# Kernel optimization log

Hardware: AMD Instinct MI355X
Metric: run time of the kernel (lower is better)

The kernel has to match this reference:

```python
import jax, jax.numpy as jnp
import numpy as np

B, L, H, S, EXP = 8, 2048, 256, 64, 2
E = H * EXP

def setup_inputs() -> dict:
    key = jax.random.key(0)
    ks = jax.random.split(key, 12)
    u = jax.random.normal(ks[0], (B, L, H), dtype=jnp.float32)
    W_in = jax.random.normal(ks[1], (H, 2 * E), dtype=jnp.float32) * 0.02
    b_in = jax.random.normal(ks[2], (2 * E,), dtype=jnp.float32) * 0.02
    conv_w = jax.random.normal(ks[3], (E, 3), dtype=jnp.float32) * 0.3  # depthwise k=3
    conv_b = jax.random.normal(ks[4], (E,), dtype=jnp.float32) * 0.02
    W_x = jax.random.normal(ks[5], (E, 3 * S), dtype=jnp.float32) * 0.02
    b_x = jax.random.normal(ks[6], (3 * S,), dtype=jnp.float32) * 0.02
    A_log = jax.random.normal(ks[7], (S,), dtype=jnp.float32) * 0.1
    Dp = jnp.ones((E,), dtype=jnp.float32)
    W_out = jax.random.normal(ks[8], (E, H), dtype=jnp.float32) * 0.02
    b_out = jax.random.normal(ks[9], (H,), dtype=jnp.float32) * 0.02
    ln_g = jnp.ones((E,), dtype=jnp.float32)
    ln_b = jnp.zeros((E,), dtype=jnp.float32)
    return {"u": u, "W_in": W_in, "b_in": b_in, "conv_w": conv_w, "conv_b": conv_b,
            "W_x": W_x, "b_x": b_x, "A_log": A_log, "Dp": Dp,
            "W_out": W_out, "b_out": b_out, "ln_g": ln_g, "ln_b": ln_b}

def reference(u, W_in, b_in, conv_w, conv_b, W_x, b_x, A_log, Dp, W_out, b_out, ln_g, ln_b):
    Bb, Ll, Hh = u.shape
    Ss = A_log.shape[0]
    Ee = Dp.shape[0]
    xz = u @ W_in + b_in                      # [B,L,2E]
    x, z = jnp.split(xz, 2, axis=-1)          # [B,L,E] each
    # depthwise conv1d, kernel=3, padding=1 along L
    xp = jnp.pad(x, ((0, 0), (1, 1), (0, 0)))
    x = xp[:, :-2] * conv_w[:, 0] + xp[:, 1:-1] * conv_w[:, 1] + xp[:, 2:] * conv_w[:, 2] + conv_b
    x = jax.nn.silu(x)
    ssm = x @ W_x + b_x                       # [B,L,3S]
    delta, Bm, Cm = jnp.split(ssm, 3, axis=-1)
    delta = jax.nn.softplus(delta)            # [B,L,S]
    A = -jnp.exp(jnp.clip(A_log, -5.0, 5.0))  # [S]
    # torch broadcast quirk: delta[...,None] * A[None,None,:] -> [B,L,S,S], entry = delta[b,l,i]*A[j]
    A_d = jnp.exp(jnp.clip(delta[:, :, :, None] * A[None, None, None, :], -10.0, 0.0))  # [B,L,S,S]
    # bmm(B_discrete, x[:,t,:,None]) == (delta*B) * sum_e x, broadcast over E
    inp_term = (delta * Bm) * x.sum(-1, keepdims=True)  # [B,L,S]

    def step(h, inputs):
        A_t, it_t, C_t, x_t = inputs          # [B,S,S],[B,S],[B,S],[B,E]
        h = jnp.einsum('bij,bje->bie', A_t, h) + it_t[:, :, None]
        h = jnp.clip(h, -100.0, 100.0)
        y = jnp.einsum('bse,bs->be', h, C_t) + Dp * x_t
        return h, y

    h0 = jnp.zeros((Bb, Ss, Ee), dtype=u.dtype)
    xs = (jnp.swapaxes(A_d, 0, 1), jnp.swapaxes(inp_term, 0, 1),
          jnp.swapaxes(Cm, 0, 1), jnp.swapaxes(x, 0, 1))
    _, ys = jax.lax.scan(step, h0, xs)
    outputs = jnp.swapaxes(ys, 0, 1)          # [B,L,E]
    mu = outputs.mean(-1, keepdims=True)
    var = ((outputs - mu) ** 2).mean(-1, keepdims=True)
    y = (outputs - mu) / jnp.sqrt(var + 1e-5) * ln_g + ln_b
    y = y * jax.nn.silu(z)
    return y @ W_out + b_out  # dropout is identity in eval mode
```

## Files before the change

### kernel.cpp

```cpp
#include <hip/hip_runtime.h>
#include <hip/hip_bf16.h>

constexpr int BB = 8;
constexpr int LLEN = 2048;
constexpr int HH = 256;
constexpr int EE = 512;
constexpr int MM = BB * LLEN;

typedef short bf16x8 __attribute__((ext_vector_type(8)));
typedef float f32x4  __attribute__((ext_vector_type(4)));

static __device__ inline unsigned short f2bf(float f) {
    unsigned u = __builtin_bit_cast(unsigned, f);
    unsigned r = (u + 0x7FFFu + ((u >> 16) & 1u)) >> 16;
    return (unsigned short)r;
}
static __device__ inline float bf2f(unsigned short h) {
    return __builtin_bit_cast(float, (unsigned)h << 16);
}

#define GL2LDS(gp, lp) __builtin_amdgcn_global_load_lds( \
    (const __attribute__((address_space(1))) void*)(gp), \
    (__attribute__((address_space(3))) void*)(lp), 16, 0, 0)

__global__ __launch_bounds__(256) void cast_bf16_kernel(
    const float* __restrict__ in, unsigned short* __restrict__ out)
{
    int b = blockIdx.x;
    int cpx = gridDim.x >> 3;
    int lin = (b & 7) * cpx + (b >> 3);
    int i = (lin * 256 + threadIdx.x) * 4;
    float4 v = *reinterpret_cast<const float4*>(in + i);
    ushort4 o = {f2bf(v.x), f2bf(v.y), f2bf(v.z), f2bf(v.w)};
    *reinterpret_cast<ushort4*>(out + i) = o;
}

__global__ __launch_bounds__(256) void transpose_cast_kernel(
    const float* __restrict__ W, unsigned short* __restrict__ Wt, int K, int N)
{
    int i = blockIdx.x * 256 + threadIdx.x;
    if (i < K * N) {
        int n = i / K, k = i - n * K;
        Wt[i] = f2bf(W[(size_t)k * N + n]);
    }
}

__global__ __launch_bounds__(256) void k1_gemm(
    const unsigned short* __restrict__ A, const unsigned short* __restrict__ Bt,
    const float* __restrict__ bias,
    unsigned short* __restrict__ xb, unsigned short* __restrict__ zsb)
{
    __shared__ unsigned short Al[128 * 64];
    __shared__ unsigned short Bl[128 * 64];

    const int tid = threadIdx.x;
    const int lane = tid & 63;
    const int wave = tid >> 6;
    const int wrow = wave >> 1, wcol = wave & 1;
    const int l15 = lane & 15;
    const int lk  = lane >> 4;

    const int cpx = gridDim.x >> 3;
    int lin = blockIdx.x;
    lin = (lin & 7) * cpx + (lin >> 3);
    const int row0 = (lin >> 3) * 128;
    const int col0 = (lin & 7) * 128;
    const bool zside = col0 >= EE;
    unsigned short* Cp = zside ? zsb : xb;
    const int cb = zside ? col0 - EE : col0;

    f32x4 acc[4][4] = {};

    #pragma unroll
    for (int t = 0; t < 4; ++t) {
        const int kt = t * 64;
        #pragma unroll
        for (int i = 0; i < 4; ++i) {
            int sid = i * 256 + tid;
            int r = sid >> 3, sl = sid & 7;
            GL2LDS(A + (size_t)(row0 + r) * 256 + kt + ((sl ^ (r & 7)) << 3),
                   &Al[sid * 8]);
        }
        #pragma unroll
        for (int i = 0; i < 4; ++i) {
            int sid = i * 256 + tid;
            int r = sid >> 3, sl = sid & 7;
            GL2LDS(Bt + (size_t)(col0 + r) * 256 + kt + ((sl ^ (r & 7)) << 3),
                   &Bl[sid * 8]);
        }
        asm volatile("s_waitcnt vmcnt(0)" ::: "memory");
        __builtin_amdgcn_sched_barrier(0);
        __builtin_amdgcn_s_barrier();

        bf16x8 af[4][2], bfr[4][2];
        #pragma unroll
        for (int m = 0; m < 4; ++m) {
            const int r = wrow * 64 + m * 16 + l15;
            #pragma unroll
            for (int kk = 0; kk < 2; ++kk) {
                const int sl = (kk * 4 + lk) ^ (r & 7);
                af[m][kk] = *reinterpret_cast<const bf16x8*>(&Al[r * 64 + sl * 8]);
            }
        }
        #pragma unroll
        for (int n = 0; n < 4; ++n) {
            const int r = wcol * 64 + n * 16 + l15;
            #pragma unroll
            for (int kk = 0; kk < 2; ++kk) {
                const int sl = (kk * 4 + lk) ^ (r & 7);
                bfr[n][kk] = *reinterpret_cast<const bf16x8*>(&Bl[r * 64 + sl * 8]);
            }
        }
        #pragma unroll
        for (int kk = 0; kk < 2; ++kk)
            #pragma unroll
            for (int m = 0; m < 4; ++m)
                #pragma unroll
                for (int n = 0; n < 4; ++n)
                    acc[m][n] = __builtin_amdgcn_mfma_f32_16x16x32_bf16(
                        af[m][kk], bfr[n][kk], acc[m][n], 0, 0, 0);

        __builtin_amdgcn_s_barrier();
    }

    #pragma unroll
    for (int m = 0; m < 4; ++m) {
        #pragma unroll
        for (int n = 0; n < 4; ++n) {
            const int colloc = wcol * 64 + n * 16 + l15;
            const float bv = bias[col0 + colloc];
            #pragma unroll
            for (int i = 0; i < 4; ++i) {
                const int row = row0 + wrow * 64 + m * 16 + lk * 4 + i;
                float v = acc[m][n][i] + bv;
                if (zside) v = v / (1.f + __expf(-v));
                Cp[(size_t)row * EE + cb + colloc] = f2bf(v);
            }
        }
    }
}

__global__ __launch_bounds__(256, 1) void kb_mid_gemm3(
    const unsigned short* __restrict__ xb, const unsigned short* __restrict__ zsb,
    const unsigned short* __restrict__ Bt,
    const float* __restrict__ bias, float* __restrict__ out,
    const float* __restrict__ conv_w, const float* __restrict__ conv_b,
    const float* __restrict__ Dp, const float* __restrict__ ln_g,
    const float* __restrict__ ln_b)
{
    __shared__ unsigned short G[64 * 512];
    __shared__ unsigned short Bl[64 * 512];

    const int tid = threadIdx.x;
    const int lane = tid & 63;
    const int wave = tid >> 6;
    const int l15 = lane & 15;
    const int lk  = lane >> 4;

    const int b = blockIdx.x;
    const int lin = (b & 7) * 32 + (b >> 3);
    const int r0 = lin * 64;

    #pragma unroll
    for (int i = 0; i < 16; ++i) {
        int id = i * 256 + tid;
        int r = id >> 6, s = id & 63;
        GL2LDS(Bt + (size_t)r * 512 + ((s ^ (r & 7)) << 3), &Bl[id * 8]);
    }

    const int e0 = lane * 8;
    float cw0[8], cw1[8], cw2[8], cb8[8], dp8[8], lg8[8], lb8[8];
    #pragma unroll
    for (int j = 0; j < 8; ++j) {
        int e = e0 + j;
        cw0[j] = conv_w[e * 3 + 0];
        cw1[j] = conv_w[e * 3 + 1];
        cw2[j] = conv_w[e * 3 + 2];
        cb8[j] = conv_b[e];
        dp8[j] = Dp[e];
        lg8[j] = ln_g[e];
        lb8[j] = ln_b[e];
    }

    for (int it = 0; it < 16; ++it) {
        const int i = wave * 16 + it;
        const int gr = r0 + i;
        const int l = gr & (LLEN - 1);
        const size_t base = (size_t)gr * EE + e0;

        bf16x8 xc = *reinterpret_cast<const bf16x8*>(xb + base);
        bf16x8 xm = {}, xp = {};
        if (l > 0)        xm = *reinterpret_cast<const bf16x8*>(xb + base - EE);
        if (l < LLEN - 1) xp = *reinterpret_cast<const bf16x8*>(xb + base + EE);
        bf16x8 zv = *reinterpret_cast<const bf16x8*>(zsb + base);

        float o[8];
        float s1 = 0.f, s2 = 0.f;
        #pragma unroll
        for (int j = 0; j < 8; ++j) {
            float v = cb8[j]
                    + bf2f((unsigned short)xm[j]) * cw0[j]
                    + bf2f((unsigned short)xc[j]) * cw1[j]
                    + bf2f((unsigned short)xp[j]) * cw2[j];
            float sx = v / (1.f + __expf(-v));
            float oe = dp8[j] * sx;
            o[j] = oe;
            s1 += oe;
            s2 += oe * oe;
        }
        #pragma unroll
        for (int off = 1; off < 64; off <<= 1) {
            s1 += __shfl_xor(s1, off);
            s2 += __shfl_xor(s2, off);
        }
        const float mu  = s1 * (1.f / EE);
        const float var = s2 * (1.f / EE) - mu * mu;
        const float inv = rsqrtf(var + 1e-5f);

        bf16x8 gv;
        #pragma unroll
        for (int j = 0; j < 8; ++j) {
            float gy = ((o[j] - mu) * inv * lg8[j] + lb8[j]) * bf2f((unsigned short)zv[j]);
            gv[j] = (short)f2bf(gy);
        }
        *reinterpret_cast<bf16x8*>(&G[i * 512 + ((lane ^ (i & 7)) << 3)]) = gv;
    }
    __syncthreads();

    const int wrow = wave >> 1, wcol = wave & 1;
    for (int c = 0; c < 4; ++c) {
        f32x4 acc[2][2] = {};
        #pragma unroll
        for (int ks = 0; ks < 16; ++ks) {
            bf16x8 af[2], bfr[2];
            #pragma unroll
            for (int m = 0; m < 2; ++m) {
                const int ra = wrow * 32 + m * 16 + l15;
                const int ph = (ks * 4 + lk) ^ (ra & 7);
                af[m] = *reinterpret_cast<const bf16x8*>(&G[ra * 512 + ph * 8]);
            }
            #pragma unroll
            for (int n = 0; n < 2; ++n) {
                const int rb = wcol * 32 + n * 16 + l15;
                const int ph = (ks * 4 + lk) ^ (rb & 7);
                bfr[n] = *reinterpret_cast<const bf16x8*>(&Bl[rb * 512 + ph * 8]);
            }
            #pragma unroll
            for (int m = 0; m < 2; ++m)
                #pragma unroll
                for (int n = 0; n < 2; ++n)
                    acc[m][n] = __builtin_amdgcn_mfma_f32_16x16x32_bf16(
                        af[m], bfr[n], acc[m][n], 0, 0, 0);
        }
        #pragma unroll
        for (int m = 0; m < 2; ++m) {
            #pragma unroll
            for (int n = 0; n < 2; ++n) {
                int col = c * 64 + wcol * 32 + n * 16 + l15;
                float bv = bias[col];
                #pragma unroll
                for (int i = 0; i < 4; ++i) {
                    int row = r0 + wrow * 32 + m * 16 + lk * 4 + i;
                    out[(size_t)row * HH + col] = acc[m][n][i] + bv;
                }
            }
        }
        if (c < 3) {
            __syncthreads();
            #pragma unroll
            for (int i = 0; i < 16; ++i) {
                int id = i * 256 + tid;
                int r = id >> 6, s = id & 63;
                GL2LDS(Bt + (size_t)((c + 1) * 64 + r) * 512 + ((s ^ (r & 7)) << 3),
                       &Bl[id * 8]);
            }
            __syncthreads();
        }
    }
}

extern "C" void kernel_launch(void* const* d_in, const int* in_sizes, int n_in,
                              void* d_out, int out_size, void* d_ws, size_t ws_size,
                              hipStream_t stream)
{
    const float* u      = (const float*)d_in[0];
    const float* W_in   = (const float*)d_in[1];
    const float* b_in   = (const float*)d_in[2];
    const float* conv_w = (const float*)d_in[3];
    const float* conv_b = (const float*)d_in[4];
    const float* Dp     = (const float*)d_in[8];
    const float* W_out  = (const float*)d_in[9];
    const float* b_out  = (const float*)d_in[10];
    const float* ln_g   = (const float*)d_in[11];
    const float* ln_b   = (const float*)d_in[12];
    float* out = (float*)d_out;

    char* ws = (char*)d_ws;
    unsigned short* ubf   = (unsigned short*)ws; ws += (size_t)MM * HH * 2;
    unsigned short* wtin  = (unsigned short*)ws; ws += (size_t)1024 * HH * 2;
    unsigned short* wtout = (unsigned short*)ws; ws += (size_t)HH * EE * 2;
    unsigned short* xbuf  = (unsigned short*)ws; ws += (size_t)MM * EE * 2;
    unsigned short* zsbuf = (unsigned short*)ws;

    dim3 blk(256);

    transpose_cast_kernel<<<dim3((1024 * HH + 255) / 256), blk, 0, stream>>>(W_in, wtin, HH, 1024);
    transpose_cast_kernel<<<dim3((HH * EE + 255) / 256), blk, 0, stream>>>(W_out, wtout, EE, HH);
    cast_bf16_kernel<<<dim3(MM * HH / 1024), blk, 0, stream>>>(u, ubf);

    k1_gemm<<<dim3(1024), blk, 0, stream>>>(ubf, wtin, b_in, xbuf, zsbuf);

    kb_mid_gemm3<<<dim3(256), blk, 0, stream>>>(
        xbuf, zsbuf, wtout, b_out, out, conv_w, conv_b, Dp, ln_g, ln_b);
}
```

Baseline: 64.97 us.

## Stage GEMM epilogue through LDS and store x/z in column-panel layout

The first GEMM's epilogue now writes its bf16 results into LDS, two 64-row halves at a time, and then emits coalesced 16-byte stores. The global layout of xb and zsb changes from row-major [M,512] to four column panels of [M,128], so each block writes one contiguous panel. The consuming mid kernel is updated to index the panel layout, including the neighbour-row reads for the conv. This replaces scattered 2-byte global stores with wide, coalesced ones, at the cost of extra barriers and an LDS round trip.

```diff
diff --git a/kernel.cpp b/kernel.cpp
--- a/kernel.cpp
+++ b/kernel.cpp
@@ -50,8 +50,9 @@
     const float* __restrict__ bias,
     unsigned short* __restrict__ xb, unsigned short* __restrict__ zsb)
 {
-    __shared__ unsigned short Al[128 * 64];
-    __shared__ unsigned short Bl[128 * 64];
+    __shared__ __align__(16) unsigned short lds[2 * 128 * 64];
+    unsigned short* Al = lds;
+    unsigned short* Bl = lds + 128 * 64;
 
     const int tid = threadIdx.x;
     const int lane = tid & 63;
@@ -66,8 +67,6 @@
     const int row0 = (lin >> 3) * 128;
     const int col0 = (lin & 7) * 128;
     const bool zside = col0 >= EE;
-    unsigned short* Cp = zside ? zsb : xb;
-    const int cb = zside ? col0 - EE : col0;
 
     f32x4 acc[4][4] = {};
 
@@ -123,19 +122,39 @@
         __builtin_amdgcn_s_barrier();
     }
 
+    const int p = (zside ? (col0 - EE) : col0) >> 7;
+    unsigned short* panel = (zside ? zsb : xb) + (size_t)p * ((size_t)MM * 128);
+    unsigned short* Ep = lds;
+
     #pragma unroll
-    for (int m = 0; m < 4; ++m) {
-        #pragma unroll
-        for (int n = 0; n < 4; ++n) {
-            const int colloc = wcol * 64 + n * 16 + l15;
-            const float bv = bias[col0 + colloc];
-            #pragma unroll
-            for (int i = 0; i < 4; ++i) {
-                const int row = row0 + wrow * 64 + m * 16 + lk * 4 + i;
-                float v = acc[m][n][i] + bv;
-                if (zside) v = v / (1.f + __expf(-v));
-                Cp[(size_t)row * EE + cb + colloc] = f2bf(v);
-            }
+    for (int rnd = 0; rnd < 2; ++rnd) {
+        __syncthreads();
+        if (wrow == rnd) {
+            #pragma unroll
+            for (int m = 0; m < 4; ++m) {
+                #pragma unroll
+                for (int n = 0; n < 4; ++n) {
+                    const int colloc = wcol * 64 + n * 16 + l15;
+                    const float bv = bias[col0 + colloc];
+                    #pragma unroll
+                    for (int i = 0; i < 4; ++i) {
+                        const int lrow = m * 16 + lk * 4 + i;
+                        float v = acc[m][n][i] + bv;
+                        if (zside) v = v / (1.f + __expf(-v));
+                        Ep[lrow * 132 + colloc] = f2bf(v);
+                    }
+                }
+            }
+        }
+        __syncthreads();
+        {
+            const int row = tid >> 2, q = tid & 3;
+            const unsigned short* sp = &Ep[row * 132 + q * 32];
+            unsigned short* gp = panel + (size_t)(row0 + rnd * 64 + row) * 128 + q * 32;
+            #pragma unroll
+            for (int j = 0; j < 4; ++j)
+                *reinterpret_cast<bf16x8*>(gp + j * 8) =
+                    *reinterpret_cast<const bf16x8*>(sp + j * 8);
         }
     }
 }
@@ -169,6 +188,8 @@
     }
 
     const int e0 = lane * 8;
+    const size_t pst = (size_t)MM * 128;
+    const size_t poff = (size_t)(lane >> 4) * pst + (e0 & 127);
     float cw0[8], cw1[8], cw2[8], cb8[8], dp8[8], lg8[8], lb8[8];
     #pragma unroll
     for (int j = 0; j < 8; ++j) {
@@ -186,12 +207,12 @@
         const int i = wave * 16 + it;
         const int gr = r0 + i;
         const int l = gr & (LLEN - 1);
-        const size_t base = (size_t)gr * EE + e0;
+        const size_t base = poff + (size_t)gr * 128;
 
         bf16x8 xc = *reinterpret_cast<const bf16x8*>(xb + base);
         bf16x8 xm = {}, xp = {};
-        if (l > 0)        xm = *reinterpret_cast<const bf16x8*>(xb + base - EE);
-        if (l < LLEN - 1) xp = *reinterpret_cast<const bf16x8*>(xb + base + EE);
+        if (l > 0)        xm = *reinterpret_cast<const bf16x8*>(xb + base - 128);
+        if (l < LLEN - 1) xp = *reinterpret_cast<const bf16x8*>(xb + base + 128);
         bf16x8 zv = *reinterpret_cast<const bf16x8*>(zsb + base);
 
         float o[8];
```

After: 76.87 us. 18.3% more time.

## Shrink k1 K-tile and prefetch W_out chunks through registers in output GEMM

Applied to the files above, without the earlier changes.

The first GEMM now steps K in chunks of 32 with unswizzled LDS tiles half the size, using plain __syncthreads instead of the manual barriers. The output GEMM no longer issues direct global-to-LDS loads for W_out. It loads each next chunk into registers while the current chunk's MFMAs run, then writes it into swizzled LDS after a barrier. The goal is to overlap weight fetch with compute and lower LDS use for occupancy. The costs are more registers, more barrier rounds in k1, and possible bank conflicts from the dropped swizzle.

```diff
diff --git a/kernel.cpp b/kernel.cpp
--- a/kernel.cpp
+++ b/kernel.cpp
@@ -50,8 +50,8 @@
     const float* __restrict__ bias,
     unsigned short* __restrict__ xb, unsigned short* __restrict__ zsb)
 {
-    __shared__ unsigned short Al[128 * 64];
-    __shared__ unsigned short Bl[128 * 64];
+    __shared__ unsigned short Al[128 * 32];
+    __shared__ unsigned short Bl[128 * 32];
 
     const int tid = threadIdx.x;
     const int lane = tid & 63;
@@ -72,55 +72,42 @@
     f32x4 acc[4][4] = {};
 
     #pragma unroll
-    for (int t = 0; t < 4; ++t) {
-        const int kt = t * 64;
-        #pragma unroll
-        for (int i = 0; i < 4; ++i) {
+    for (int t = 0; t < 8; ++t) {
+        const int kt = t * 32;
+        #pragma unroll
+        for (int i = 0; i < 2; ++i) {
             int sid = i * 256 + tid;
-            int r = sid >> 3, sl = sid & 7;
-            GL2LDS(A + (size_t)(row0 + r) * 256 + kt + ((sl ^ (r & 7)) << 3),
-                   &Al[sid * 8]);
-        }
-        #pragma unroll
-        for (int i = 0; i < 4; ++i) {
+            int r = sid >> 2, o = sid & 3;
+            GL2LDS(A + (size_t)(row0 + r) * 256 + kt + o * 8, &Al[sid * 8]);
+        }
+        #pragma unroll
+        for (int i = 0; i < 2; ++i) {
             int sid = i * 256 + tid;
-            int r = sid >> 3, sl = sid & 7;
-            GL2LDS(Bt + (size_t)(col0 + r) * 256 + kt + ((sl ^ (r & 7)) << 3),
-                   &Bl[sid * 8]);
+            int r = sid >> 2, o = sid & 3;
+            GL2LDS(Bt + (size_t)(col0 + r) * 256 + kt + o * 8, &Bl[sid * 8]);
         }
         asm volatile("s_waitcnt vmcnt(0)" ::: "memory");
-        __builtin_amdgcn_sched_barrier(0);
-        __builtin_amdgcn_s_barrier();
-
-        bf16x8 af[4][2], bfr[4][2];
+        __syncthreads();
+
+        bf16x8 af[4], bfr[4];
         #pragma unroll
         for (int m = 0; m < 4; ++m) {
             const int r = wrow * 64 + m * 16 + l15;
-            #pragma unroll
-            for (int kk = 0; kk < 2; ++kk) {
-                const int sl = (kk * 4 + lk) ^ (r & 7);
-                af[m][kk] = *reinterpret_cast<const bf16x8*>(&Al[r * 64 + sl * 8]);
-            }
+            af[m] = *reinterpret_cast<const bf16x8*>(&Al[r * 32 + lk * 8]);
         }
         #pragma unroll
         for (int n = 0; n < 4; ++n) {
             const int r = wcol * 64 + n * 16 + l15;
-            #pragma unroll
-            for (int kk = 0; kk < 2; ++kk) {
-                const int sl = (kk * 4 + lk) ^ (r & 7);
-                bfr[n][kk] = *reinterpret_cast<const bf16x8*>(&Bl[r * 64 + sl * 8]);
-            }
-        }
-        #pragma unroll
-        for (int kk = 0; kk < 2; ++kk)
-            #pragma unroll
-            for (int m = 0; m < 4; ++m)
-                #pragma unroll
-                for (int n = 0; n < 4; ++n)
-                    acc[m][n] = __builtin_amdgcn_mfma_f32_16x16x32_bf16(
-                        af[m][kk], bfr[n][kk], acc[m][n], 0, 0, 0);
-
-        __builtin_amdgcn_s_barrier();
+            bfr[n] = *reinterpret_cast<const bf16x8*>(&Bl[r * 32 + lk * 8]);
+        }
+        #pragma unroll
+        for (int m = 0; m < 4; ++m)
+            #pragma unroll
+            for (int n = 0; n < 4; ++n)
+                acc[m][n] = __builtin_amdgcn_mfma_f32_16x16x32_bf16(
+                    af[m], bfr[n], acc[m][n], 0, 0, 0);
+
+        __syncthreads();
     }
 
     #pragma unroll
@@ -160,13 +147,6 @@
     const int b = blockIdx.x;
     const int lin = (b & 7) * 32 + (b >> 3);
     const int r0 = lin * 64;
-
-    #pragma unroll
-    for (int i = 0; i < 16; ++i) {
-        int id = i * 256 + tid;
-        int r = id >> 6, s = id & 63;
-        GL2LDS(Bt + (size_t)r * 512 + ((s ^ (r & 7)) << 3), &Bl[id * 8]);
-    }
 
     const int e0 = lane * 8;
     float cw0[8], cw1[8], cw2[8], cb8[8], dp8[8], lg8[8], lb8[8];
@@ -225,10 +205,31 @@
         }
         *reinterpret_cast<bf16x8*>(&G[i * 512 + ((lane ^ (i & 7)) << 3)]) = gv;
     }
+
+    bf16x8 breg[16];
+    #pragma unroll
+    for (int i = 0; i < 16; ++i) {
+        int id = i * 256 + tid;
+        breg[i] = *reinterpret_cast<const bf16x8*>(Bt + (size_t)id * 8);
+    }
+    __syncthreads();
+    #pragma unroll
+    for (int i = 0; i < 16; ++i) {
+        int id = i * 256 + tid;
+        int r = id >> 6, s = id & 63;
+        *reinterpret_cast<bf16x8*>(&Bl[r * 512 + ((s ^ (r & 7)) << 3)]) = breg[i];
+    }
     __syncthreads();
 
     const int wrow = wave >> 1, wcol = wave & 1;
     for (int c = 0; c < 4; ++c) {
+        if (c < 3) {
+            #pragma unroll
+            for (int i = 0; i < 16; ++i) {
+                int id = (c + 1) * 4096 + i * 256 + tid;
+                breg[i] = *reinterpret_cast<const bf16x8*>(Bt + (size_t)id * 8);
+            }
+        }
         f32x4 acc[2][2] = {};
         #pragma unroll
         for (int ks = 0; ks < 16; ++ks) {
@@ -271,8 +272,7 @@
             for (int i = 0; i < 16; ++i) {
                 int id = i * 256 + tid;
                 int r = id >> 6, s = id & 63;
-                GL2LDS(Bt + (size_t)((c + 1) * 64 + r) * 512 + ((s ^ (r & 7)) << 3),
-                       &Bl[id * 8]);
+                *reinterpret_cast<bf16x8*>(&Bl[r * 512 + ((s ^ (r & 7)) << 3)]) = breg[i];
             }
             __syncthreads();
         }
```

Result: slower. 66.32 us (+2.1%).
